# Optimization experiments

Measured on AMD Instinct MI355X. Metric: run time of the kernel, lower is better.

The kernel has to match this reference:

```python
import jax, jax.numpy as jnp
import numpy as np


def _cdist_p2(x, y):
    # x: [B, N, D], y: [B, M, D] -> [B, N, M] euclidean distances
    x2 = jnp.sum(x * x, axis=-1, keepdims=True)          # [B, N, 1]
    y2 = jnp.sum(y * y, axis=-1, keepdims=True)          # [B, M, 1]
    xy = jnp.einsum('bnd,bmd->bnm', x, y)                # [B, N, M]
    d2 = x2 + jnp.swapaxes(y2, -1, -2) - 2.0 * xy
    return jnp.sqrt(jnp.maximum(d2, 0.0))


def setup_inputs() -> dict:
    key = jax.random.key(0)
    kx, ky = jax.random.split(key)
    B, N, M, D = 8, 8192, 8192, 64
    x = jax.random.normal(kx, (B, N, D), dtype=jnp.float32)
    y = jax.random.normal(ky, (B, M, D), dtype=jnp.float32)
    return {"x": x, "y": y}


def reference(x, y):
    # relative_distances: [B, N, M]
    rd = _cdist_p2(x, y)
    M = rd.shape[-1]
    a = jnp.min(rd, axis=-1)            # [B, N] nearest y for each x
    b = jnp.min(rd, axis=-2)            # [B, M] nearest x for each y
    loss_per_batch = jnp.sum(a, axis=-1) + jnp.sum(b, axis=-1)  # [B]
    return jnp.mean(loss_per_batch) / M
```

## Files before the change

kernel.cpp:

```cpp
#include <hip/hip_runtime.h>
#include <cstdint>
#include <cstddef>

typedef unsigned short u16;
typedef __attribute__((ext_vector_type(8))) short short8;
typedef __attribute__((ext_vector_type(8))) u16 ushort8;
typedef __attribute__((ext_vector_type(4))) float float4_t;

#define BB 8
#define NN 8192
#define DD 64
#define NTILES 64
#define TILE_SHORTS 8192
#define LDS_STRIDE 68

__device__ inline u16 f32_to_bf16(float f) {
  unsigned u = __float_as_uint(f);
  u += 0x7FFFu + ((u >> 16) & 1u);
  return (u16)(u >> 16);
}

__device__ inline unsigned enc_ord(float f) {
  unsigned u = __float_as_uint(f);
  return (u & 0x80000000u) ? ~u : (u | 0x80000000u);
}
__device__ inline float dec_ord(unsigned u) {
  return __uint_as_float((u & 0x80000000u) ? (u & 0x7fffffffu) : ~u);
}

__global__ __launch_bounds__(256) void pre_kernel(
    const float* __restrict__ x, const float* __restrict__ y,
    u16* __restrict__ xs, u16* __restrict__ ys,
    float* __restrict__ x2h, float* __restrict__ y2h,
    unsigned* __restrict__ rowmax_u, unsigned* __restrict__ colmax_u,
    float* __restrict__ out, const int use_part)
{
  __shared__ float stage[128 * LDS_STRIDE];

  const int bid = blockIdx.x;
  const int tid = threadIdx.x;

  if (!use_part) {
    if (bid < 256)      colmax_u[(bid << 8) | tid] = 0u;
    else if (bid < 512) rowmax_u[((bid - 256) << 8) | tid] = 0u;
  }
  if (bid == 0 && tid == 0) out[0] = 0.f;

  const bool isY = bid >= 512;
  const int t = bid & 511;
  const float* src = (isY ? y : x) + (size_t)t * (128 * DD);
  u16* dst = (isY ? ys : xs) + (size_t)t * TILE_SHORTS;
  float* s2 = (isY ? y2h : x2h) + t * 128;

#pragma unroll
  for (int c = 0; c < 8; ++c) {
    const int idx = c * 256 + tid;
    float4 f = ((const float4*)src)[idx];
    const int r = idx >> 4, kc = idx & 15;
    *(float4*)&stage[r * LDS_STRIDE + kc * 4] = f;
  }
  __syncthreads();

  {
    const int r = tid >> 1, half = tid & 1;
    const float* rp = &stage[r * LDS_STRIDE + half * 32];
    float ss = 0.f;
#pragma unroll
    for (int k = 0; k < 8; ++k) {
      float4 f = *(const float4*)&rp[k * 4];
      ss += f.x*f.x + f.y*f.y + f.z*f.z + f.w*f.w;
    }
    ss += __shfl_xor(ss, 1);
    if (half == 0) s2[r] = 0.5f * ss;
  }

  {
    const int w = tid >> 6, lane = tid & 63;
    const int qq = lane >> 4, rl = lane & 15;
#pragma unroll
    for (int u = 0; u < 4; ++u) {
      const int chunk = w * 4 + u;
      const int I = chunk >> 1, s = chunk & 1;
      const float* rp = &stage[(I*16 + rl) * LDS_STRIDE + s*32 + qq*8];
      ushort8 o;
#pragma unroll
      for (int j = 0; j < 8; ++j) o[j] = f32_to_bf16(rp[j]);
      *(ushort8*)(dst + chunk*512 + lane*8) = o;
    }
  }
}

__global__ __launch_bounds__(256, 2) void main_kernel(
    const u16* __restrict__ xs, const u16* __restrict__ ys,
    const float* __restrict__ x2h, const float* __restrict__ y2h,
    float* __restrict__ rowpart, float* __restrict__ colpart,
    unsigned* __restrict__ rowmax_u, unsigned* __restrict__ colmax_u,
    const int use_part)
{
  __shared__ float rowbuf[4][128];

  const int bid = blockIdx.x;
  const int b   = bid & 7;
  const int nt  = (bid >> 3) & 63;
  const int h   = bid >> 9;
  const int mt_start = h << 5, mt_end = mt_start + 32;
  const int tid = threadIdx.x;
  const int w = tid >> 6, lane = tid & 63;
  const int l15 = lane & 15, q = lane >> 4;
  const int n0 = nt << 7;

  const u16* xs_tile = xs + (size_t)((b << 6) | nt) * TILE_SHORTS;
  short8 afr[8][2];
#pragma unroll
  for (int i = 0; i < 8; ++i)
#pragma unroll
    for (int s = 0; s < 2; ++s)
      afr[i][s] = *(const short8*)(xs_tile + (i*2 + s)*512 + lane*8);

  float4_t negx2[8];
  const float* x2b = x2h + b*NN + n0;
#pragma unroll
  for (int i = 0; i < 8; ++i) {
    float4_t v = *(const float4_t*)(x2b + i*16 + q*4);
    negx2[i] = {-v[0], -v[1], -v[2], -v[3]};
  }

  float rowmax[8][4];
#pragma unroll
  for (int i = 0; i < 8; ++i)
#pragma unroll
    for (int r = 0; r < 4; ++r) rowmax[i][r] = -3.0e38f;

  const float* y2b = y2h + b*NN;
  const u16* ys_b  = ys + (size_t)(b << 6) * TILE_SHORTS;
  float* colp      = colpart + (size_t)((b << 6) | nt) * NN;
  unsigned* colu   = colmax_u + b*NN;

  short8 bcur[2][2];
  float y2cur[2];
#pragma unroll
  for (int j = 0; j < 2; ++j) {
#pragma unroll
    for (int s = 0; s < 2; ++s)
      bcur[j][s] = *(const short8*)(ys_b + (size_t)mt_start*TILE_SHORTS
                                    + ((2*w + j)*2 + s)*512 + lane*8);
    y2cur[j] = y2b[mt_start*128 + w*32 + j*16 + l15];
  }

  for (int mt = mt_start; mt < mt_end; ++mt) {
    const int mtn = (mt + 1 < mt_end) ? (mt + 1) : mt_start;
    short8 bnext[2][2];
    float y2next[2];
    const u16* g = ys_b + (size_t)mtn * TILE_SHORTS;
#pragma unroll
    for (int j = 0; j < 2; ++j) {
#pragma unroll
      for (int s = 0; s < 2; ++s)
        bnext[j][s] = *(const short8*)(g + ((2*w + j)*2 + s)*512 + lane*8);
      y2next[j] = y2b[mtn*128 + w*32 + j*16 + l15];
    }

    float cmax[2];
#pragma unroll
    for (int j = 0; j < 2; ++j) {
      float4_t acc[8];
#pragma unroll
      for (int i = 0; i < 8; ++i)
        acc[i] = __builtin_amdgcn_mfma_f32_16x16x32_bf16(afr[i][0], bcur[j][0], negx2[i], 0, 0, 0);
#pragma unroll
      for (int i = 0; i < 8; ++i)
        acc[i] = __builtin_amdgcn_mfma_f32_16x16x32_bf16(afr[i][1], bcur[j][1], acc[i], 0, 0, 0);

      float m01 = fmaxf(fmaxf(acc[0][0], acc[0][1]), fmaxf(acc[0][2], acc[0][3]));
#pragma unroll
      for (int i = 1; i < 8; ++i) {
        float mi = fmaxf(fmaxf(acc[i][0], acc[i][1]), fmaxf(acc[i][2], acc[i][3]));
        m01 = fmaxf(m01, mi);
      }
      cmax[j] = m01;

      const float y2j = y2cur[j];
#pragma unroll
      for (int i = 0; i < 8; ++i)
#pragma unroll
        for (int r = 0; r < 4; ++r)
          rowmax[i][r] = fmaxf(rowmax[i][r], acc[i][r] - y2j);
    }

#pragma unroll
    for (int j = 0; j < 2; ++j) {
      cmax[j] = fmaxf(cmax[j], __shfl_xor(cmax[j], 16));
      cmax[j] = fmaxf(cmax[j], __shfl_xor(cmax[j], 32));
    }
    float cv = (q & 1) ? cmax[1] : cmax[0];
    const int m = (mt << 7) + w*32 + q*16 + l15;
    if (q < 2) {
      if (use_part) colp[m] = cv;
      else          atomicMax(&colu[m], enc_ord(cv));
    }

#pragma unroll
    for (int j = 0; j < 2; ++j) {
#pragma unroll
      for (int s = 0; s < 2; ++s) bcur[j][s] = bnext[j][s];
      y2cur[j] = y2next[j];
    }
  }

#pragma unroll
  for (int i = 0; i < 8; ++i)
#pragma unroll
    for (int r = 0; r < 4; ++r) {
      float v = rowmax[i][r];
      v = fmaxf(v, __shfl_xor(v, 1));
      v = fmaxf(v, __shfl_xor(v, 2));
      v = fmaxf(v, __shfl_xor(v, 4));
      v = fmaxf(v, __shfl_xor(v, 8));
      rowmax[i][r] = v;
    }
  if (l15 == 0) {
#pragma unroll
    for (int i = 0; i < 8; ++i)
#pragma unroll
      for (int r = 0; r < 4; ++r)
        rowbuf[w][i*16 + q*4 + r] = rowmax[i][r];
  }
  __syncthreads();
  if (tid < 128) {
    float v = fmaxf(fmaxf(rowbuf[0][tid], rowbuf[1][tid]),
                    fmaxf(rowbuf[2][tid], rowbuf[3][tid]));
    if (use_part) rowpart[(size_t)((h << 9) | (b << 6) | nt) * 128 + tid] = v;
    else          atomicMax(&rowmax_u[b*NN + n0 + tid], enc_ord(v));
  }
}

__global__ __launch_bounds__(256) void reduce_kernel(
    const float* __restrict__ rowpart, const float* __restrict__ colpart,
    const unsigned* __restrict__ rowmax_u, const unsigned* __restrict__ colmax_u,
    const float* __restrict__ y2h, float* __restrict__ out,
    const int use_part)
{
  const int bid = blockIdx.x;
  const int tid = threadIdx.x;
  const int g = bid*256 + tid;
  const int b = g >> 13, m = g & (NN - 1);

  float vc, vr;
  if (use_part) {
    vc = -3.0e38f;
#pragma unroll 8
    for (int nt = 0; nt < 64; ++nt)
      vc = fmaxf(vc, colpart[(size_t)((b << 6) | nt) * NN + m]);
    const int nt = m >> 7, r = m & 127;
    float r0 = rowpart[(size_t)((0 << 9) | (b << 6) | nt) * 128 + r];
    float r1 = rowpart[(size_t)((1 << 9) | (b << 6) | nt) * 128 + r];
    vr = fmaxf(r0, r1);
  } else {
    vc = dec_ord(colmax_u[g]);
    vr = dec_ord(rowmax_u[g]);
  }
  float s = sqrtf(fmaxf(2.f*(y2h[g] - vc), 0.f))
          + sqrtf(fmaxf(-2.f*vr, 0.f));

#pragma unroll
  for (int d = 1; d < 64; d <<= 1) s += __shfl_xor(s, d);
  __shared__ float wsum[4];
  if ((tid & 63) == 0) wsum[tid >> 6] = s;
  __syncthreads();
  if (tid == 0)
    atomicAdd(out, (wsum[0] + wsum[1] + wsum[2] + wsum[3]) * (1.0f / 65536.0f));
}

extern "C" void kernel_launch(void* const* d_in, const int* in_sizes, int n_in,
                              void* d_out, int out_size, void* d_ws, size_t ws_size,
                              hipStream_t stream) {
  const float* x = (const float*)d_in[0];
  const float* y = (const float*)d_in[1];
  float* out = (float*)d_out;

  char* p = (char*)d_ws;
  u16* xs = (u16*)p;            p += (size_t)512 * 16384;
  u16* ys = (u16*)p;            p += (size_t)512 * 16384;
  float* x2h = (float*)p;       p += (size_t)65536 * 4;
  float* y2h = (float*)p;       p += (size_t)65536 * 4;
  char* tail = p;
  float* colpart = (float*)tail;
  float* rowpart = (float*)(tail + (size_t)512 * 8192 * 4);
  unsigned* colmax_u = (unsigned*)tail;
  unsigned* rowmax_u = (unsigned*)(tail + (size_t)65536 * 4);
  const size_t need_part = (size_t)(tail - (char*)d_ws) +
                           (size_t)512 * 8192 * 4 + (size_t)1024 * 128 * 4;
  const int use_part = (ws_size >= need_part) ? 1 : 0;

  pre_kernel<<<dim3(1024), dim3(256), 0, stream>>>(x, y, xs, ys, x2h, y2h,
                                                   rowmax_u, colmax_u, out,
                                                   use_part);
  main_kernel<<<dim3(1024), dim3(256), 0, stream>>>(xs, ys, x2h, y2h,
                                                    rowpart, colpart,
                                                    rowmax_u, colmax_u,
                                                    use_part);
  reduce_kernel<<<dim3(256), dim3(256), 0, stream>>>(rowpart, colpart,
                                                     rowmax_u, colmax_u, y2h,
                                                     out, use_part);
}
```

Baseline: 167.5 us.

## Halve row tile to 64, double grid, raise occupancy, ping-pong B loads

Each main-kernel block now covers 64 x-rows instead of 128, so the grid doubles to 2048 blocks and launch bounds allow 3 blocks per CU. The B-fragment prefetch becomes a manually unrolled two-buffer ping-pong that avoids register copies. The change aims to raise occupancy and hide load latency. In exchange each loaded B tile feeds fewer MFMAs, and the column-partial buffer and its reduction pass double in size.

```diff
diff --git a/kernel.cpp b/kernel.cpp
--- a/kernel.cpp
+++ b/kernel.cpp
@@ -90,98 +90,91 @@
   }
 }
 
-__global__ __launch_bounds__(256, 2) void main_kernel(
+__global__ __launch_bounds__(256, 3) void main_kernel(
     const u16* __restrict__ xs, const u16* __restrict__ ys,
     const float* __restrict__ x2h, const float* __restrict__ y2h,
     float* __restrict__ rowpart, float* __restrict__ colpart,
     unsigned* __restrict__ rowmax_u, unsigned* __restrict__ colmax_u,
     const int use_part)
 {
-  __shared__ float rowbuf[4][128];
+  __shared__ float rowbuf[4][64];
 
   const int bid = blockIdx.x;
   const int b   = bid & 7;
-  const int nt  = (bid >> 3) & 63;
-  const int h   = bid >> 9;
-  const int mt_start = h << 5, mt_end = mt_start + 32;
+  const int nt  = (bid >> 3) & 127;
+  const int h   = bid >> 10;
   const int tid = threadIdx.x;
   const int w = tid >> 6, lane = tid & 63;
   const int l15 = lane & 15, q = lane >> 4;
-  const int n0 = nt << 7;
-
-  const u16* xs_tile = xs + (size_t)((b << 6) | nt) * TILE_SHORTS;
-  short8 afr[8][2];
-#pragma unroll
-  for (int i = 0; i < 8; ++i)
+  const int n0 = nt << 6;
+  const int mt_start = h << 5;
+
+  const u16* xs_tile = xs + (size_t)((b << 6) | (nt >> 1)) * TILE_SHORTS
+                       + (nt & 1) * 4096;
+  short8 afr[4][2];
+#pragma unroll
+  for (int i = 0; i < 4; ++i)
 #pragma unroll
     for (int s = 0; s < 2; ++s)
       afr[i][s] = *(const short8*)(xs_tile + (i*2 + s)*512 + lane*8);
 
-  float4_t negx2[8];
+  float4_t negx2[4];
   const float* x2b = x2h + b*NN + n0;
 #pragma unroll
-  for (int i = 0; i < 8; ++i) {
+  for (int i = 0; i < 4; ++i) {
     float4_t v = *(const float4_t*)(x2b + i*16 + q*4);
     negx2[i] = {-v[0], -v[1], -v[2], -v[3]};
   }
 
-  float rowmax[8][4];
-#pragma unroll
-  for (int i = 0; i < 8; ++i)
+  float rowmax[4][4];
+#pragma unroll
+  for (int i = 0; i < 4; ++i)
 #pragma unroll
     for (int r = 0; r < 4; ++r) rowmax[i][r] = -3.0e38f;
 
-  const float* y2b = y2h + b*NN;
-  const u16* ys_b  = ys + (size_t)(b << 6) * TILE_SHORTS;
-  float* colp      = colpart + (size_t)((b << 6) | nt) * NN;
-  unsigned* colu   = colmax_u + b*NN;
-
-  short8 bcur[2][2];
-  float y2cur[2];
-#pragma unroll
-  for (int j = 0; j < 2; ++j) {
-#pragma unroll
-    for (int s = 0; s < 2; ++s)
-      bcur[j][s] = *(const short8*)(ys_b + (size_t)mt_start*TILE_SHORTS
-                                    + ((2*w + j)*2 + s)*512 + lane*8);
-    y2cur[j] = y2b[mt_start*128 + w*32 + j*16 + l15];
-  }
-
-  for (int mt = mt_start; mt < mt_end; ++mt) {
-    const int mtn = (mt + 1 < mt_end) ? (mt + 1) : mt_start;
-    short8 bnext[2][2];
-    float y2next[2];
-    const u16* g = ys_b + (size_t)mtn * TILE_SHORTS;
+  const u16*  pB = ys + (size_t)((b << 6) + mt_start) * TILE_SHORTS
+                   + (w*4)*512 + lane*8;
+  const float* pY = y2h + b*NN + mt_start*128 + w*32 + l15;
+  float*    colp = colpart + (size_t)((b << 7) | nt) * NN;
+  unsigned* colu = colmax_u + b*NN;
+  int coff = mt_start*128 + w*32 + q*16 + l15;
+
+  short8 bA[2][2], bB[2][2];
+  float  yA[2],   yB[2];
+
+  auto loadB = [&](short8 (&B)[2][2], float (&Y)[2]) {
+    B[0][0] = *(const short8*)(pB);
+    B[0][1] = *(const short8*)(pB + 512);
+    B[1][0] = *(const short8*)(pB + 1024);
+    B[1][1] = *(const short8*)(pB + 1536);
+    Y[0] = pY[0];
+    Y[1] = pY[16];
+    pB += TILE_SHORTS;
+    pY += 128;
+  };
+
+  auto compute = [&](const short8 (&B)[2][2], const float (&Y)[2]) {
+    float cmax[2];
 #pragma unroll
     for (int j = 0; j < 2; ++j) {
-#pragma unroll
-      for (int s = 0; s < 2; ++s)
-        bnext[j][s] = *(const short8*)(g + ((2*w + j)*2 + s)*512 + lane*8);
-      y2next[j] = y2b[mtn*128 + w*32 + j*16 + l15];
-    }
-
-    float cmax[2];
-#pragma unroll
-    for (int j = 0; j < 2; ++j) {
-      float4_t acc[8];
-#pragma unroll
-      for (int i = 0; i < 8; ++i)
-        acc[i] = __builtin_amdgcn_mfma_f32_16x16x32_bf16(afr[i][0], bcur[j][0], negx2[i], 0, 0, 0);
-#pragma unroll
-      for (int i = 0; i < 8; ++i)
-        acc[i] = __builtin_amdgcn_mfma_f32_16x16x32_bf16(afr[i][1], bcur[j][1], acc[i], 0, 0, 0);
-
-      float m01 = fmaxf(fmaxf(acc[0][0], acc[0][1]), fmaxf(acc[0][2], acc[0][3]));
-#pragma unroll
-      for (int i = 1; i < 8; ++i) {
-        float mi = fmaxf(fmaxf(acc[i][0], acc[i][1]), fmaxf(acc[i][2], acc[i][3]));
-        m01 = fmaxf(m01, mi);
-      }
-      cmax[j] = m01;
-
-      const float y2j = y2cur[j];
-#pragma unroll
-      for (int i = 0; i < 8; ++i)
+      float4_t acc[4];
+#pragma unroll
+      for (int i = 0; i < 4; ++i)
+        acc[i] = __builtin_amdgcn_mfma_f32_16x16x32_bf16(afr[i][0], B[j][0], negx2[i], 0, 0, 0);
+#pragma unroll
+      for (int i = 0; i < 4; ++i)
+        acc[i] = __builtin_amdgcn_mfma_f32_16x16x32_bf16(afr[i][1], B[j][1], acc[i], 0, 0, 0);
+
+      float m0 = fmaxf(fmaxf(acc[0][0], acc[0][1]), fmaxf(acc[0][2], acc[0][3]));
+#pragma unroll
+      for (int i = 1; i < 4; ++i)
+        m0 = fmaxf(fmaxf(m0, fmaxf(acc[i][0], acc[i][1])),
+                   fmaxf(acc[i][2], acc[i][3]));
+      cmax[j] = m0;
+
+      const float y2j = Y[j];
+#pragma unroll
+      for (int i = 0; i < 4; ++i)
 #pragma unroll
         for (int r = 0; r < 4; ++r)
           rowmax[i][r] = fmaxf(rowmax[i][r], acc[i][r] - y2j);
@@ -193,22 +186,26 @@
       cmax[j] = fmaxf(cmax[j], __shfl_xor(cmax[j], 32));
     }
     float cv = (q & 1) ? cmax[1] : cmax[0];
-    const int m = (mt << 7) + w*32 + q*16 + l15;
     if (q < 2) {
-      if (use_part) colp[m] = cv;
-      else          atomicMax(&colu[m], enc_ord(cv));
-    }
-
-#pragma unroll
-    for (int j = 0; j < 2; ++j) {
-#pragma unroll
-      for (int s = 0; s < 2; ++s) bcur[j][s] = bnext[j][s];
-      y2cur[j] = y2next[j];
-    }
-  }
-
-#pragma unroll
-  for (int i = 0; i < 8; ++i)
+      if (use_part) colp[coff] = cv;
+      else          atomicMax(&colu[coff], enc_ord(cv));
+    }
+    coff += 128;
+  };
+
+  loadB(bA, yA);
+  for (int it = 0; it < 15; ++it) {
+    loadB(bB, yB);
+    compute(bA, yA);
+    loadB(bA, yA);
+    compute(bB, yB);
+  }
+  loadB(bB, yB);
+  compute(bA, yA);
+  compute(bB, yB);
+
+#pragma unroll
+  for (int i = 0; i < 4; ++i)
 #pragma unroll
     for (int r = 0; r < 4; ++r) {
       float v = rowmax[i][r];
@@ -220,16 +217,16 @@
     }
   if (l15 == 0) {
 #pragma unroll
-    for (int i = 0; i < 8; ++i)
+    for (int i = 0; i < 4; ++i)
 #pragma unroll
       for (int r = 0; r < 4; ++r)
         rowbuf[w][i*16 + q*4 + r] = rowmax[i][r];
   }
   __syncthreads();
-  if (tid < 128) {
+  if (tid < 64) {
     float v = fmaxf(fmaxf(rowbuf[0][tid], rowbuf[1][tid]),
                     fmaxf(rowbuf[2][tid], rowbuf[3][tid]));
-    if (use_part) rowpart[(size_t)((h << 9) | (b << 6) | nt) * 128 + tid] = v;
+    if (use_part) rowpart[(size_t)bid * 64 + tid] = v;
     else          atomicMax(&rowmax_u[b*NN + n0 + tid], enc_ord(v));
   }
 }
@@ -249,11 +246,11 @@
   if (use_part) {
     vc = -3.0e38f;
 #pragma unroll 8
-    for (int nt = 0; nt < 64; ++nt)
-      vc = fmaxf(vc, colpart[(size_t)((b << 6) | nt) * NN + m]);
-    const int nt = m >> 7, r = m & 127;
-    float r0 = rowpart[(size_t)((0 << 9) | (b << 6) | nt) * 128 + r];
-    float r1 = rowpart[(size_t)((1 << 9) | (b << 6) | nt) * 128 + r];
+    for (int nt = 0; nt < 128; ++nt)
+      vc = fmaxf(vc, colpart[(size_t)((b << 7) | nt) * NN + m]);
+    const int nt = m >> 6, r = m & 63;
+    float r0 = rowpart[(size_t)((0 << 10) | (nt << 3) | b) * 64 + r];
+    float r1 = rowpart[(size_t)((1 << 10) | (nt << 3) | b) * 64 + r];
     vr = fmaxf(r0, r1);
   } else {
     vc = dec_ord(colmax_u[g]);
@@ -285,17 +282,17 @@
   float* y2h = (float*)p;       p += (size_t)65536 * 4;
   char* tail = p;
   float* colpart = (float*)tail;
-  float* rowpart = (float*)(tail + (size_t)512 * 8192 * 4);
+  float* rowpart = (float*)(tail + (size_t)1024 * 8192 * 4);
   unsigned* colmax_u = (unsigned*)tail;
   unsigned* rowmax_u = (unsigned*)(tail + (size_t)65536 * 4);
   const size_t need_part = (size_t)(tail - (char*)d_ws) +
-                           (size_t)512 * 8192 * 4 + (size_t)1024 * 128 * 4;
+                           (size_t)1024 * 8192 * 4 + (size_t)2048 * 64 * 4;
   const int use_part = (ws_size >= need_part) ? 1 : 0;
 
   pre_kernel<<<dim3(1024), dim3(256), 0, stream>>>(x, y, xs, ys, x2h, y2h,
                                                    rowmax_u, colmax_u, out,
                                                    use_part);
-  main_kernel<<<dim3(1024), dim3(256), 0, stream>>>(xs, ys, x2h, y2h,
+  main_kernel<<<dim3(2048), dim3(256), 0, stream>>>(xs, ys, x2h, y2h,
                                                     rowpart, colpart,
                                                     rowmax_u, colmax_u,
                                                     use_part);
```

Result: slower. 307.1 us (+83.3%).
